# Kernel optimization log

Hardware: AMD Instinct MI355X
Metric: run time of the kernel (lower is better)

## Reference

```python
import jax, jax.numpy as jnp
import numpy as np

HIDDEN_SIZE = 1152
OUTPUT_LENGTH = 256
POSITIONS_PAD_VALUE = -1
GRID = 64  # 64x64 patch grid -> seq_len 4096


def setup_inputs() -> dict:
    key = jax.random.key(0)
    k1, k2 = jax.random.split(key)
    B, S, H = 8, GRID * GRID, HIDDEN_SIZE
    hidden_states = jax.random.normal(k1, (B, S, H), dtype=jnp.float32)
    positions_xy = jax.random.randint(k2, (B, S, 2), 0, GRID, dtype=jnp.int32)
    return {"hidden_states": hidden_states, "positions_xy": positions_xy}


def _pool(hidden_states, positions_xy):
    B, S, H = hidden_states.shape
    L = OUTPUT_LENGTH
    k = int(np.sqrt(S // L))
    assert k * k * L == S
    root = float(np.sqrt(HIDDEN_SIZE))

    padding = jnp.all(positions_xy == POSITIONS_PAD_VALUE, axis=-1)      # [B,S]
    safe = jnp.maximum(positions_xy, 0)                                   # [B,S,2]
    max_x = jnp.max(safe[..., 0], axis=-1, keepdims=True) + 1            # [B,1]
    kern = safe // k                                                      # [B,S,2]
    flat = kern[..., 0] + (max_x // k) * kern[..., 1]                     # [B,S] bin id in [0,L)
    w = jnp.where(padding, 0.0, 1.0 / float(k * k))                       # [B,S]

    def pool_one(xb, idxb, wb):
        # scatter-mean: equivalent to one-hot(idx)^T @ x with 1/k^2 weights
        pooled = jax.ops.segment_sum(xb * wb[:, None], idxb, num_segments=L)  # [L,H]
        wsum = jax.ops.segment_sum(wb, idxb, num_segments=L)                  # [L]
        return pooled, wsum > 0

    pooled, mask = jax.vmap(pool_one)(hidden_states.astype(jnp.float32), flat, w)
    pooled = pooled.astype(hidden_states.dtype) * root
    return pooled, mask


def reference(hidden_states, positions_xy):
    pooled, mask = _pool(hidden_states, positions_xy)
    return (pooled, mask)
```

## Files before the change

kernel.cpp:

```cpp
#include <hip/hip_runtime.h>

#define HD 1152
#define SQ 4096
#define NB 256
#define BT 8
#define KK 4

__global__ void k_maxx(const int* __restrict__ pos, int* __restrict__ maxx) {
    int b = blockIdx.x;
    int tid = threadIdx.x;
    const int* p = pos + (size_t)b * SQ * 2;
    int m = 0;
    for (int i = tid; i < SQ; i += 256) {
        int x = p[2 * i];
        if (x < 0) x = 0;
        m = max(m, x);
    }
    for (int off = 32; off > 0; off >>= 1)
        m = max(m, __shfl_down(m, off, 64));
    __shared__ int sm[4];
    if ((tid & 63) == 0) sm[tid >> 6] = m;
    __syncthreads();
    if (tid == 0) {
        m = max(max(sm[0], sm[1]), max(sm[2], sm[3]));
        maxx[b] = m + 1;
    }
}

__global__ void k_flat(const int* __restrict__ pos, const int* __restrict__ maxx,
                       int* __restrict__ flat) {
    int idx = blockIdx.x * 256 + threadIdx.x;
    if (idx >= BT * SQ) return;
    int b = idx >> 12;
    int2 xy = ((const int2*)pos)[idx];
    bool pad = (xy.x == -1) && (xy.y == -1);
    int sx = xy.x < 0 ? 0 : xy.x;
    int sy = xy.y < 0 ? 0 : xy.y;
    int f = (sx / KK) + (maxx[b] / KK) * (sy / KK);
    flat[idx] = pad ? -1 : f;
}

__global__ void __launch_bounds__(256) k_pool(const float* __restrict__ hs,
                                              const int* __restrict__ flat,
                                              float* __restrict__ out,
                                              float* __restrict__ mask) {
    int bl = blockIdx.x;
    int b = bl >> 8;
    int l = bl & (NB - 1);
    int tid = threadIdx.x;
    int wv = tid >> 6, lane = tid & 63;

    __shared__ unsigned short list[SQ];
    __shared__ int wcnt[4];

    const int* f = flat + b * SQ;
    const int base = wv * (SQ / 4);
    const unsigned long long lanemask = (1ull << lane) - 1ull;

    int cnt = 0;
    for (int c = 0; c < SQ / 4; c += 64) {
        bool m = (f[base + c + lane] == l);
        cnt += __popcll(__ballot(m));
    }
    if (lane == 0) wcnt[wv] = cnt;
    __syncthreads();

    int off = 0;
    #pragma unroll
    for (int w = 0; w < 4; ++w) if (w < wv) off += wcnt[w];
    int total = wcnt[0] + wcnt[1] + wcnt[2] + wcnt[3];

    for (int c = 0; c < SQ / 4; c += 64) {
        bool m = (f[base + c + lane] == l);
        unsigned long long bal = __ballot(m);
        if (m) list[off + __popcll(bal & lanemask)] = (unsigned short)(base + c + lane);
        off += __popcll(bal);
    }
    __syncthreads();

    float4 a0 = make_float4(0.f, 0.f, 0.f, 0.f);
    float4 a1 = make_float4(0.f, 0.f, 0.f, 0.f);
    for (int i = 0; i < total; ++i) {
        int s = list[i];
        const float4* row = (const float4*)(hs + ((size_t)b * SQ + s) * HD);
        float4 v0 = row[tid];
        a0.x += v0.x; a0.y += v0.y; a0.z += v0.z; a0.w += v0.w;
        if (tid < HD / 4 - 256) {
            float4 v1 = row[256 + tid];
            a1.x += v1.x; a1.y += v1.y; a1.z += v1.z; a1.w += v1.w;
        }
    }

    const float scale = 2.1213203435596424f;
    float4* o = (float4*)(out + (size_t)bl * HD);
    a0.x *= scale; a0.y *= scale; a0.z *= scale; a0.w *= scale;
    o[tid] = a0;
    if (tid < HD / 4 - 256) {
        a1.x *= scale; a1.y *= scale; a1.z *= scale; a1.w *= scale;
        o[256 + tid] = a1;
    }
    if (tid == 0) mask[bl] = (total > 0) ? 1.0f : 0.0f;
}

extern "C" void kernel_launch(void* const* d_in, const int* in_sizes, int n_in,
                              void* d_out, int out_size, void* d_ws, size_t ws_size,
                              hipStream_t stream) {
    const float* hs = (const float*)d_in[0];
    const int* pos = (const int*)d_in[1];
    float* out = (float*)d_out;
    float* mask = out + (size_t)BT * NB * HD;

    int* maxx = (int*)d_ws;
    int* flat = maxx + 16;

    k_maxx<<<BT, 256, 0, stream>>>(pos, maxx);
    k_flat<<<(BT * SQ) / 256, 256, 0, stream>>>(pos, maxx, flat);
    k_pool<<<BT * NB, 256, 0, stream>>>(hs, flat, out, mask);
}
```

Before: 39.93 us.

## Fuse maxx and flat-index kernels, use 16-bit bin ids and vectorized list build

Merges the max-x reduction and bin-id computation into one 1024-thread kernel per batch, which removes a launch. Bin ids are stored as 16-bit values, halving the index traffic. The pool kernel now loads 16 ids per lane with vector loads and builds its compacted token list from a shuffle prefix scan instead of two ballot passes. The accumulation loop is unrolled by two rows to keep more loads in flight. Padding now maps to 0xFFFF, which never equals a valid bin.

```diff
diff --git a/kernel.cpp b/kernel.cpp
--- a/kernel.cpp
+++ b/kernel.cpp
@@ -6,88 +6,118 @@
 #define BT 8
 #define KK 4
 
-__global__ void k_maxx(const int* __restrict__ pos, int* __restrict__ maxx) {
+__global__ void __launch_bounds__(1024) k_prep(const int* __restrict__ pos,
+                                               unsigned short* __restrict__ flat) {
     int b = blockIdx.x;
     int tid = threadIdx.x;
-    const int* p = pos + (size_t)b * SQ * 2;
-    int m = 0;
-    for (int i = tid; i < SQ; i += 256) {
-        int x = p[2 * i];
-        if (x < 0) x = 0;
-        m = max(m, x);
-    }
+    const int4* p = (const int4*)(pos + (size_t)b * SQ * 2);
+    int4 a = p[2 * tid];
+    int4 c = p[2 * tid + 1];
+
+    int mx = max(max(a.x, a.z), max(c.x, c.z));
+    if (mx < 0) mx = 0;
     for (int off = 32; off > 0; off >>= 1)
-        m = max(m, __shfl_down(m, off, 64));
-    __shared__ int sm[4];
-    if ((tid & 63) == 0) sm[tid >> 6] = m;
+        mx = max(mx, __shfl_down(mx, off, 64));
+    __shared__ int sm[16];
+    if ((tid & 63) == 0) sm[tid >> 6] = mx;
     __syncthreads();
     if (tid == 0) {
-        m = max(max(sm[0], sm[1]), max(sm[2], sm[3]));
-        maxx[b] = m + 1;
+        int v = sm[0];
+        #pragma unroll
+        for (int i = 1; i < 16; ++i) v = max(v, sm[i]);
+        sm[0] = v;
     }
-}
+    __syncthreads();
+    const int mxq = (sm[0] + 1) / KK;
 
-__global__ void k_flat(const int* __restrict__ pos, const int* __restrict__ maxx,
-                       int* __restrict__ flat) {
-    int idx = blockIdx.x * 256 + threadIdx.x;
-    if (idx >= BT * SQ) return;
-    int b = idx >> 12;
-    int2 xy = ((const int2*)pos)[idx];
-    bool pad = (xy.x == -1) && (xy.y == -1);
-    int sx = xy.x < 0 ? 0 : xy.x;
-    int sy = xy.y < 0 ? 0 : xy.y;
-    int f = (sx / KK) + (maxx[b] / KK) * (sy / KK);
-    flat[idx] = pad ? -1 : f;
+    #define FLATID(X, Y) ((unsigned short)((((X) == -1) && ((Y) == -1)) ? 0xFFFFu \
+        : (unsigned)((max((X), 0) / KK) + mxq * (max((Y), 0) / KK))))
+    ushort4 o;
+    o.x = FLATID(a.x, a.y);
+    o.y = FLATID(a.z, a.w);
+    o.z = FLATID(c.x, c.y);
+    o.w = FLATID(c.z, c.w);
+    ((ushort4*)flat)[(size_t)b * (SQ / 4) + tid] = o;
+    #undef FLATID
 }
 
 __global__ void __launch_bounds__(256) k_pool(const float* __restrict__ hs,
-                                              const int* __restrict__ flat,
+                                              const unsigned short* __restrict__ flat,
                                               float* __restrict__ out,
                                               float* __restrict__ mask) {
     int bl = blockIdx.x;
     int b = bl >> 8;
-    int l = bl & (NB - 1);
+    unsigned l = (unsigned)(bl & (NB - 1));
     int tid = threadIdx.x;
     int wv = tid >> 6, lane = tid & 63;
 
     __shared__ unsigned short list[SQ];
     __shared__ int wcnt[4];
 
-    const int* f = flat + b * SQ;
-    const int base = wv * (SQ / 4);
-    const unsigned long long lanemask = (1ull << lane) - 1ull;
+    const int tokbase = wv * 1024 + lane * 16;
+    const unsigned short* f = flat + b * SQ;
+    const uint4* fp = (const uint4*)(f + tokbase);
+    uint4 q0 = fp[0];
+    uint4 q1 = fp[1];
 
-    int cnt = 0;
-    for (int c = 0; c < SQ / 4; c += 64) {
-        bool m = (f[base + c + lane] == l);
-        cnt += __popcll(__ballot(m));
+    unsigned w[8] = {q0.x, q0.y, q0.z, q0.w, q1.x, q1.y, q1.z, q1.w};
+    unsigned m16 = 0;
+    #pragma unroll
+    for (int j = 0; j < 8; ++j) {
+        if ((w[j] & 0xFFFFu) == l) m16 |= 1u << (2 * j);
+        if ((w[j] >> 16) == l)     m16 |= 1u << (2 * j + 1);
     }
-    if (lane == 0) wcnt[wv] = cnt;
+    int cnt = __popc(m16);
+
+    int pre = cnt;
+    #pragma unroll
+    for (int off = 1; off < 64; off <<= 1) {
+        int n = __shfl_up(pre, off, 64);
+        if (lane >= off) pre += n;
+    }
+    if (lane == 63) wcnt[wv] = pre;
+    int excl = pre - cnt;
     __syncthreads();
 
-    int off = 0;
+    int woff = 0;
     #pragma unroll
-    for (int w = 0; w < 4; ++w) if (w < wv) off += wcnt[w];
+    for (int v = 0; v < 4; ++v) if (v < wv) woff += wcnt[v];
     int total = wcnt[0] + wcnt[1] + wcnt[2] + wcnt[3];
 
-    for (int c = 0; c < SQ / 4; c += 64) {
-        bool m = (f[base + c + lane] == l);
-        unsigned long long bal = __ballot(m);
-        if (m) list[off + __popcll(bal & lanemask)] = (unsigned short)(base + c + lane);
-        off += __popcll(bal);
+    int r = woff + excl;
+    unsigned m = m16;
+    while (m) {
+        int j = __ffs(m) - 1;
+        m &= m - 1;
+        list[r++] = (unsigned short)(tokbase + j);
     }
     __syncthreads();
 
     float4 a0 = make_float4(0.f, 0.f, 0.f, 0.f);
     float4 a1 = make_float4(0.f, 0.f, 0.f, 0.f);
-    for (int i = 0; i < total; ++i) {
-        int s = list[i];
-        const float4* row = (const float4*)(hs + ((size_t)b * SQ + s) * HD);
-        float4 v0 = row[tid];
+    const float* hb = hs + (size_t)b * SQ * HD;
+    int i = 0;
+    for (; i + 1 < total; i += 2) {
+        const float4* r0 = (const float4*)(hb + (size_t)list[i] * HD);
+        const float4* r1 = (const float4*)(hb + (size_t)list[i + 1] * HD);
+        float4 v0 = r0[tid];
+        float4 v1 = r1[tid];
+        a0.x += v0.x; a0.y += v0.y; a0.z += v0.z; a0.w += v0.w;
+        a0.x += v1.x; a0.y += v1.y; a0.z += v1.z; a0.w += v1.w;
+        if (tid < HD / 4 - 256) {
+            float4 u0 = r0[256 + tid];
+            float4 u1 = r1[256 + tid];
+            a1.x += u0.x; a1.y += u0.y; a1.z += u0.z; a1.w += u0.w;
+            a1.x += u1.x; a1.y += u1.y; a1.z += u1.z; a1.w += u1.w;
+        }
+    }
+    if (i < total) {
+        const float4* r0 = (const float4*)(hb + (size_t)list[i] * HD);
+        float4 v0 = r0[tid];
         a0.x += v0.x; a0.y += v0.y; a0.z += v0.z; a0.w += v0.w;
         if (tid < HD / 4 - 256) {
-            float4 v1 = row[256 + tid];
-            a1.x += v1.x; a1.y += v1.y; a1.z += v1.z; a1.w += v1.w;
+            float4 u0 = r0[256 + tid];
+            a1.x += u0.x; a1.y += u0.y; a1.z += u0.z; a1.w += u0.w;
         }
     }
 
@@ -110,10 +140,8 @@
     float* out = (float*)d_out;
     float* mask = out + (size_t)BT * NB * HD;
 
-    int* maxx = (int*)d_ws;
-    int* flat = maxx + 16;
+    unsigned short* flat = (unsigned short*)d_ws;
 
-    k_maxx<<<BT, 256, 0, stream>>>(pos, maxx);
-    k_flat<<<(BT * SQ) / 256, 256, 0, stream>>>(pos, maxx, flat);
+    k_prep<<<BT, 1024, 0, stream>>>(pos, flat);
     k_pool<<<BT * NB, 256, 0, stream>>>(hs, flat, out, mask);
 }
```

Result: faster. 35.90 us (-10.1%).
